# Kernel tuning notes

Measured on AMD Instinct MI355X. Metric: run time of the kernel, lower is better.

## Reference

```python
import jax, jax.numpy as jnp
import numpy as np


def _log_g(x):
    # log of g(x) = where(x>=0, x+0.5, sigmoid(x)), computed stably in log-space
    return jnp.where(x >= 0, jnp.log(jax.nn.relu(x) + 0.5), -jax.nn.softplus(-x))


def setup_inputs() -> dict:
    key = jax.random.key(0)
    k1, k2, k3, k4, k5 = jax.random.split(key, 5)
    B, T, D, E = 4, 4096, 1024, 2048  # batch, seq, dim, exp_dim (expansion 2.0)
    x = jax.random.normal(k1, (B, T, D), dtype=jnp.float32)
    log_h_0 = jax.random.normal(k2, (B, 1, E), dtype=jnp.float32)
    # torch Linear(dim, 2*exp_dim): store transposed weight [D, 2E] for x @ w_f
    w_f = jax.random.normal(k3, (D, 2 * E), dtype=jnp.float32) * (1.0 / np.sqrt(D))
    b_f = jax.random.normal(k4, (2 * E,), dtype=jnp.float32) * 0.01
    # torch Linear(exp_dim, dim, bias=False): stored as [E, D] for h_t @ w_down
    w_down = jax.random.normal(k5, (E, D), dtype=jnp.float32) * (1.0 / np.sqrt(E))
    return {"x": x, "log_h_0": log_h_0, "w_f": w_f, "b_f": b_f, "w_down": w_down}


def reference(x, log_h_0, w_f, b_f, w_down):
    # fused gate/candidate projection: [B,T,2E]
    proj = jnp.einsum("btd,de->bte", x, w_f) + b_f
    k, h_x = jnp.split(proj, 2, axis=-1)  # each [B,T,E]
    log_z = -jax.nn.softplus(-k)          # log sigmoid(k)
    log_coeffs = -jax.nn.softplus(k)      # log (1 - sigmoid(k))
    log_tilde_h = _log_g(h_x)
    # prepend initial state: log_values [B,T+1,E]
    log_values = jnp.concatenate([log_h_0, log_tilde_h + log_z], axis=1)
    # a_star = pad(cumsum(log_coeffs), one leading zero along time) -> [B,T+1,E]
    a_star = jnp.pad(jnp.cumsum(log_coeffs, axis=1), ((0, 0), (1, 0), (0, 0)))
    # log-space parallel scan
    log_h = a_star + jax.lax.cumlogsumexp(log_values - a_star, axis=1)
    h_t = jnp.exp(log_h)[:, 1:]  # [B,T,E]
    h = jnp.einsum("bte,ed->btd", h_t, w_down)  # down projection (dropout p=0 -> identity)
    return h, jnp.log(h_t[:, 2:-1:3])
```

## Files before the change

### kernel.cpp

```cpp
#include <hip/hip_runtime.h>
#include <cstdint>
#include <cstddef>

typedef __attribute__((ext_vector_type(4))) float f32x4;
typedef __attribute__((ext_vector_type(8))) short short8;

__device__ __forceinline__ unsigned short f2bf(float f) {
  unsigned int u = __float_as_uint(f);
  u += 0x7fffu + ((u >> 16) & 1u);
  return (unsigned short)(u >> 16);
}
__device__ __forceinline__ float bf2f(unsigned short h) {
  return __uint_as_float(((unsigned int)h) << 16);
}
__device__ __forceinline__ float bflo(unsigned int w) {
  return __uint_as_float(w << 16);
}
__device__ __forceinline__ float bfhi(unsigned int w) {
  return __uint_as_float(w & 0xffff0000u);
}

__device__ __forceinline__ void gload16(const unsigned short* g, unsigned short* l) {
  __builtin_amdgcn_global_load_lds(
      (const __attribute__((address_space(1))) void*)g,
      (__attribute__((address_space(3))) void*)l, 16, 0, 0);
}

__global__ __launch_bounds__(256) void k_prep(const float* __restrict__ x,
                                              unsigned short* __restrict__ xhi,
                                              const float* __restrict__ wf,
                                              unsigned short* __restrict__ wfh,
                                              const float* __restrict__ wd,
                                              unsigned short* __restrict__ wdt,
                                              const float* __restrict__ bfv,
                                              float2* __restrict__ bfi) {
  int blk = blockIdx.x;
  if (blk < 16384) {
    size_t i = ((size_t)blk * 256 + threadIdx.x) * 4;
    float4 v = *(const float4*)(x + i);
    *(ushort4*)(xhi + i) = make_ushort4(f2bf(v.x), f2bf(v.y), f2bf(v.z), f2bf(v.w));
    return;
  }
  blk -= 16384;
  if (blk < 4096) {
    __shared__ float tile[32][33];
    int tx = threadIdx.x & 31, ty = threadIdx.x >> 5;
    int bx = blk & 127, by = blk >> 7;
    int c0 = bx * 32, r0 = by * 32;
#pragma unroll
    for (int i = 0; i < 4; ++i)
      tile[ty + 8 * i][tx] = wf[(size_t)(r0 + ty + 8 * i) * 4096 + (c0 + tx)];
    __syncthreads();
#pragma unroll
    for (int i = 0; i < 4; ++i) {
      int j = c0 + ty + 8 * i;
      int r = (j < 2048) ? (2 * j) : (2 * (j - 2048) + 1);
      wfh[(size_t)r * 1024 + (r0 + tx)] = f2bf(tile[tx][ty + 8 * i]);
    }
    return;
  }
  blk -= 4096;
  if (blk < 2048) {
    __shared__ float tile[32][33];
    int tx = threadIdx.x & 31, ty = threadIdx.x >> 5;
    int bx = blk & 31, by = blk >> 5;
    int c0 = bx * 32, r0 = by * 32;
#pragma unroll
    for (int i = 0; i < 4; ++i)
      tile[ty + 8 * i][tx] = wd[(size_t)(r0 + ty + 8 * i) * 1024 + (c0 + tx)];
    __syncthreads();
#pragma unroll
    for (int i = 0; i < 4; ++i)
      wdt[(size_t)(c0 + ty + 8 * i) * 2048 + (r0 + tx)] = f2bf(tile[tx][ty + 8 * i]);
    return;
  }
  blk -= 2048;
  int i = blk * 256 + threadIdx.x;
  if (i < 2048) bfi[i] = make_float2(bfv[i], bfv[2048 + i]);
}

template<bool BF16OUT>
__global__ __launch_bounds__(512, 2) void k_gemm(const unsigned short* __restrict__ A,
                                                 const unsigned short* __restrict__ B,
                                                 void* __restrict__ Cv, int M, int N, int K) {
  __shared__ unsigned short lds[65536];
  const int tid = threadIdx.x, wave = tid >> 6, lane = tid & 63;
  const size_t row0 = (size_t)blockIdx.x * 256;
  const size_t col0 = (size_t)blockIdx.y * 256;
  const int wr = wave >> 2, wc = wave & 3;
  const int r16 = lane & 15;
  const int ksw = (lane >> 4) ^ ((r16 >> 1) & 3);
  const int aoff = (wr * 128 + r16) * 32 + ksw * 8;
  const int boff = 8192 + (wc * 64 + r16) * 32 + ksw * 8;
  const int gchunk = (tid & 3) ^ ((tid >> 3) & 3);

  f32x4 acc[8][4];
#pragma unroll
  for (int i = 0; i < 8; ++i)
#pragma unroll
    for (int j = 0; j < 4; ++j) acc[i][j] = (f32x4){0.f, 0.f, 0.f, 0.f};

  auto SREG = [&](int b, int arr, int inst, int kt) {
    const unsigned short* src = arr ? B : A;
    size_t grow = (arr ? col0 : row0) + (size_t)(inst * 128 + (tid >> 2));
    gload16(src + grow * (size_t)K + (size_t)(kt * 32 + gchunk * 8),
            &lds[(b << 14) + arr * 8192 + inst * 4096 + wave * 512]);
  };

#pragma unroll
  for (int t = 0; t < 3; ++t) {
    SREG(t, 0, 0, t); SREG(t, 0, 1, t);
    SREG(t, 1, 0, t); SREG(t, 1, 1, t);
  }

  const int nT = K >> 5;
  for (int u = 0; u < nT; ++u) {
    const unsigned short* buf = &lds[(u & 3) << 14];
    const int sb = (u + 3) & 3;
    const bool pf = (u + 3 < nT);
    const int rem = nT - 1 - u;
    if (rem >= 2)      asm volatile("s_waitcnt vmcnt(8)" ::: "memory");
    else if (rem == 1) asm volatile("s_waitcnt vmcnt(4)" ::: "memory");
    else               asm volatile("s_waitcnt vmcnt(0)" ::: "memory");
    asm volatile("s_barrier" ::: "memory");
    short8 a4[4], b4[4];
#pragma unroll
    for (int nb = 0; nb < 4; ++nb)
      b4[nb] = *(const short8*)&buf[boff + nb * 512];
#pragma unroll
    for (int mb = 0; mb < 4; ++mb)
      a4[mb] = *(const short8*)&buf[aoff + mb * 512];
    if (pf) { SREG(sb, 0, 0, u + 3); SREG(sb, 1, 0, u + 3); }
    __builtin_amdgcn_s_setprio(1);
#pragma unroll
    for (int mb = 0; mb < 4; ++mb)
#pragma unroll
      for (int nb = 0; nb < 4; ++nb)
        acc[mb][nb] = __builtin_amdgcn_mfma_f32_16x16x32_bf16(a4[mb], b4[nb], acc[mb][nb], 0, 0, 0);
    __builtin_amdgcn_s_setprio(0);
#pragma unroll
    for (int mb = 0; mb < 4; ++mb)
      a4[mb] = *(const short8*)&buf[aoff + (4 + mb) * 512];
    if (pf) { SREG(sb, 0, 1, u + 3); SREG(sb, 1, 1, u + 3); }
    __builtin_amdgcn_s_setprio(1);
#pragma unroll
    for (int mb = 0; mb < 4; ++mb)
#pragma unroll
      for (int nb = 0; nb < 4; ++nb)
        acc[4 + mb][nb] = __builtin_amdgcn_mfma_f32_16x16x32_bf16(a4[mb], b4[nb], acc[4 + mb][nb], 0, 0, 0);
    __builtin_amdgcn_s_setprio(0);
  }

#pragma unroll
  for (int m = 0; m < 8; ++m)
#pragma unroll
    for (int n = 0; n < 4; ++n) {
      size_t row = row0 + wr * 128 + m * 16 + (lane >> 4) * 4;
      size_t col = col0 + wc * 64 + n * 16 + r16;
      if (BF16OUT) {
        unsigned short* C = (unsigned short*)Cv;
#pragma unroll
        for (int r = 0; r < 4; ++r) C[(row + r) * (size_t)N + col] = f2bf(acc[m][n][r]);
      } else {
        float* C = (float*)Cv;
#pragma unroll
        for (int r = 0; r < 4; ++r) C[(row + r) * (size_t)N + col] = acc[m][n][r];
      }
    }
}

#define SB 4
#define ST 4096
#define SE 2048
#define CHUNK 64
#define NCHUNK 64
#define NCHAIN (SB * SE)

__device__ __forceinline__ void transform_lin(float k, float hx, float& c, float& v) {
  float e = __expf(-k);
  float r = __builtin_amdgcn_rcpf(1.f + e);
  c = e * r;
  float e2 = __expf(-hx);
  float sg = __builtin_amdgcn_rcpf(1.f + e2);
  float g = (hx >= 0.f) ? (hx + 0.5f) : sg;
  v = r * g;
}

__global__ __launch_bounds__(256) void k_scan1(const unsigned int* __restrict__ proj32,
                                               const float2* __restrict__ bfi,
                                               float* __restrict__ Ac,
                                               float* __restrict__ Bc) {
  int idx = blockIdx.x * 256 + threadIdx.x;
  int e = idx & (SE - 1), b = (idx >> 11) & 3, c = idx >> 13;
  const float2 bb = bfi[e];
  float A = 1.f, S = 0.f;
  size_t base = ((size_t)(b * ST + c * CHUNK)) * SE + e;
  for (int i = 0; i < CHUNK; ++i) {
    unsigned int w = proj32[base];
    float cc, vv;
    transform_lin(bflo(w) + bb.x, bfhi(w) + bb.y, cc, vv);
    A *= cc;
    S = fmaf(cc, S, vv);
    base += SE;
  }
  int chain = b * SE + e;
  Ac[(size_t)c * NCHAIN + chain] = A;
  Bc[(size_t)c * NCHAIN + chain] = S;
}

__global__ __launch_bounds__(256) void k_scan2(const float* __restrict__ lh0,
                                               const float* __restrict__ Ac,
                                               const float* __restrict__ Bc,
                                               float* __restrict__ Hin) {
  int chain = blockIdx.x * 256 + threadIdx.x;
  float H = __expf(lh0[chain]);
  for (int c = 0; c < NCHUNK; ++c) {
    Hin[(size_t)c * NCHAIN + chain] = H;
    H = fmaf(Ac[(size_t)c * NCHAIN + chain], H, Bc[(size_t)c * NCHAIN + chain]);
  }
}

__global__ __launch_bounds__(256) void k_scan3(const unsigned int* __restrict__ proj32,
                                               const float2* __restrict__ bfi,
                                               const float* __restrict__ Hin,
                                               unsigned short* __restrict__ ht,
                                               float* __restrict__ out2) {
  int idx = blockIdx.x * 256 + threadIdx.x;
  int e = idx & (SE - 1), b = (idx >> 11) & 3, c = idx >> 13;
  const float2 bb = bfi[e];
  float S = Hin[(size_t)c * NCHAIN + b * SE + e];
  size_t base = ((size_t)(b * ST + c * CHUNK)) * SE + e;
  int t = c * CHUNK;
  size_t hto = ((size_t)(b * ST + t)) * SE + e;
  for (int i = 0; i < CHUNK; ++i, ++t) {
    unsigned int w = proj32[base];
    float cc, vv;
    transform_lin(bflo(w) + bb.x, bfhi(w) + bb.y, cc, vv);
    S = fmaf(cc, S, vv);
    ht[hto] = f2bf(S);
    if (t >= 2 && ((t - 2) % 3) == 0) {
      int j = (t - 2) / 3;
      out2[((size_t)b * 1365 + j) * SE + e] = __logf(S);
    }
    base += SE;
    hto += SE;
  }
}

extern "C" void kernel_launch(void* const* d_in, const int* in_sizes, int n_in,
                              void* d_out, int out_size, void* d_ws, size_t ws_size,
                              hipStream_t stream) {
  const float* x   = (const float*)d_in[0];
  const float* lh0 = (const float*)d_in[1];
  const float* wf  = (const float*)d_in[2];
  const float* bfv = (const float*)d_in[3];
  const float* wd  = (const float*)d_in[4];
  float* out1 = (float*)d_out;
  float* out2 = out1 + (size_t)SB * ST * 1024;

  char* p = (char*)d_ws;
  unsigned short* proj = (unsigned short*)p; p += 16384ull * 4096 * 2;
  unsigned short* xhi  = (unsigned short*)p; p += 16384ull * 1024 * 2;
  unsigned short* wfh  = (unsigned short*)p; p += 4096ull * 1024 * 2;
  unsigned short* wdt  = (unsigned short*)p; p += 1024ull * 2048 * 2;
  unsigned short* ht   = (unsigned short*)p; p += 16384ull * 2048 * 2;
  float* Ac            = (float*)p;          p += 64ull * 8192 * 4;
  float* Bc            = (float*)p;          p += 64ull * 8192 * 4;
  float* Hin           = (float*)p;          p += 64ull * 8192 * 4;
  float2* bfi          = (float2*)p;         p += 2048ull * 8;

  hipLaunchKernelGGL(k_prep, dim3(16384 + 4096 + 2048 + 8), dim3(256), 0, stream,
                     x, xhi, wf, wfh, wd, wdt, bfv, bfi);
  hipLaunchKernelGGL((k_gemm<true>), dim3(64, 16), dim3(512), 0, stream,
                     xhi, wfh, (void*)proj, 16384, 4096, 1024);
  hipLaunchKernelGGL(k_scan1, dim3(2048), dim3(256), 0, stream,
                     (const unsigned int*)proj, bfi, Ac, Bc);
  hipLaunchKernelGGL(k_scan2, dim3(32), dim3(256), 0, stream, lh0, Ac, Bc, Hin);
  hipLaunchKernelGGL(k_scan3, dim3(2048), dim3(256), 0, stream,
                     (const unsigned int*)proj, bfi, Hin, ht, out2);
  hipLaunchKernelGGL((k_gemm<false>), dim3(64, 4), dim3(512), 0, stream,
                     ht, wdt, (void*)out1, 16384, 1024, 2048);
}
```

Measured before the change: 309.0 us.

## Software-pipeline LDS fragment loads one K-step ahead with double-buffered registers

Restructures the GEMM main loop so that the next K-tile's A/B fragments are read from LDS into a second register set while the current tile's MFMAs run. The loop is unrolled by two to ping-pong the register buffers. The barrier and wait move to just after the next tile is issued, and all four global-to-LDS prefetches are issued together. This is meant to hide LDS read latency behind MFMA work, at the cost of more VGPRs. It also assumes nT is even and relies on the ring buffer of four LDS stages for correctness.

Result: no change. 314.2 us (+1.7%).

```diff
diff --git a/kernel.cpp b/kernel.cpp
--- a/kernel.cpp
+++ b/kernel.cpp
@@ -112,43 +112,57 @@
     SREG(t, 0, 0, t); SREG(t, 0, 1, t);
     SREG(t, 1, 0, t); SREG(t, 1, 1, t);
   }
-
   const int nT = K >> 5;
-  for (int u = 0; u < nT; ++u) {
+  asm volatile("s_waitcnt vmcnt(8)" ::: "memory");
+  asm volatile("s_barrier" ::: "memory");
+
+  short8 bA[4], a1A[4], bB[4], a1B[4];
+#pragma unroll
+  for (int nb = 0; nb < 4; ++nb) bA[nb] = *(const short8*)&lds[boff + nb * 512];
+#pragma unroll
+  for (int mb = 0; mb < 4; ++mb) a1A[mb] = *(const short8*)&lds[aoff + mb * 512];
+
+  auto ITER = [&](int u, short8 (&bc)[4], short8 (&a1c)[4],
+                  short8 (&bn)[4], short8 (&a1n)[4]) {
     const unsigned short* buf = &lds[(u & 3) << 14];
-    const int sb = (u + 3) & 3;
-    const bool pf = (u + 3 < nT);
-    const int rem = nT - 1 - u;
-    if (rem >= 2)      asm volatile("s_waitcnt vmcnt(8)" ::: "memory");
-    else if (rem == 1) asm volatile("s_waitcnt vmcnt(4)" ::: "memory");
-    else               asm volatile("s_waitcnt vmcnt(0)" ::: "memory");
-    asm volatile("s_barrier" ::: "memory");
-    short8 a4[4], b4[4];
-#pragma unroll
-    for (int nb = 0; nb < 4; ++nb)
-      b4[nb] = *(const short8*)&buf[boff + nb * 512];
+    short8 a2[4];
 #pragma unroll
     for (int mb = 0; mb < 4; ++mb)
-      a4[mb] = *(const short8*)&buf[aoff + mb * 512];
-    if (pf) { SREG(sb, 0, 0, u + 3); SREG(sb, 1, 0, u + 3); }
+      a2[mb] = *(const short8*)&buf[aoff + (4 + mb) * 512];
+    if (u + 1 < nT) {
+      if (u + 2 < nT) asm volatile("s_waitcnt vmcnt(4)" ::: "memory");
+      else            asm volatile("s_waitcnt vmcnt(0)" ::: "memory");
+      asm volatile("s_barrier" ::: "memory");
+      if (u + 3 < nT) {
+        const int sb = (u + 3) & 3;
+        SREG(sb, 0, 0, u + 3); SREG(sb, 0, 1, u + 3);
+        SREG(sb, 1, 0, u + 3); SREG(sb, 1, 1, u + 3);
+      }
+      const unsigned short* nbf = &lds[((u + 1) & 3) << 14];
+#pragma unroll
+      for (int nb = 0; nb < 4; ++nb) bn[nb] = *(const short8*)&nbf[boff + nb * 512];
+#pragma unroll
+      for (int mb = 0; mb < 4; ++mb) a1n[mb] = *(const short8*)&nbf[aoff + mb * 512];
+    }
     __builtin_amdgcn_s_setprio(1);
 #pragma unroll
     for (int mb = 0; mb < 4; ++mb)
 #pragma unroll
       for (int nb = 0; nb < 4; ++nb)
-        acc[mb][nb] = __builtin_amdgcn_mfma_f32_16x16x32_bf16(a4[mb], b4[nb], acc[mb][nb], 0, 0, 0);
+        acc[mb][nb] = __builtin_amdgcn_mfma_f32_16x16x32_bf16(a1c[mb], bc[nb], acc[mb][nb], 0, 0, 0);
     __builtin_amdgcn_s_setprio(0);
+    __builtin_amdgcn_s_setprio(1);
 #pragma unroll
     for (int mb = 0; mb < 4; ++mb)
-      a4[mb] = *(const short8*)&buf[aoff + (4 + mb) * 512];
-    if (pf) { SREG(sb, 0, 1, u + 3); SREG(sb, 1, 1, u + 3); }
-    __builtin_amdgcn_s_setprio(1);
-#pragma unroll
-    for (int mb = 0; mb < 4; ++mb)
 #pragma unroll
       for (int nb = 0; nb < 4; ++nb)
-        acc[4 + mb][nb] = __builtin_amdgcn_mfma_f32_16x16x32_bf16(a4[mb], b4[nb], acc[4 + mb][nb], 0, 0, 0);
+        acc[4 + mb][nb] = __builtin_amdgcn_mfma_f32_16x16x32_bf16(a2[mb], bc[nb], acc[4 + mb][nb], 0, 0, 0);
     __builtin_amdgcn_s_setprio(0);
+  };
+
+  for (int u = 0; u < nT; u += 2) {
+    ITER(u, bA, a1A, bB, a1B);
+    ITER(u + 1, bB, a1B, bA, a1A);
   }
 
 #pragma unroll
```
